# Kernel optimization log

Hardware: AMD Instinct MI355X
Metric: run time of the kernel (lower is better)

## Reference

```python
import jax, jax.numpy as jnp
import numpy as np

SEQ_LEN = 2048
NUM_HEADS = 16
BATCH = 2
HEAD_DIM = 64


def setup_inputs() -> dict:
    key = jax.random.key(0)
    k_q, k_e1, k_e2 = jax.random.split(key, 3)
    q = jax.random.normal(k_q, (BATCH * NUM_HEADS, SEQ_LEN, HEAD_DIM), dtype=jnp.float32)
    e1 = jax.random.normal(k_e1, (SEQ_LEN, NUM_HEADS), dtype=jnp.float32)
    e2 = jax.random.normal(k_e2, (SEQ_LEN - 1, NUM_HEADS), dtype=jnp.float32)
    return {"q": q, "e1": e1, "e2": e2}


def reference(q, e1, e2):
    # The original double loop of overwriting scatters reduces to:
    #   ret[i, j] = e1[i - j]      if i >= j   (delta = i - j in [0, S-1])
    #   ret[i, j] = e2[j - i - 1]  if j > i    (j - i - 1 in [0, S-2])
    seq_len = e1.shape[0]
    num_heads = e1.shape[1]
    batch_x_heads = q.shape[0]
    batch_dim = batch_x_heads // num_heads

    i = jnp.arange(seq_len)[:, None]
    j = jnp.arange(seq_len)[None, :]
    delta = i - j  # (S, S)
    idx1 = jnp.clip(delta, 0, seq_len - 1)
    idx2 = jnp.clip(-delta - 1, 0, seq_len - 2)
    # (S, S, H): gather from e1 below/on diagonal, e2 above diagonal
    bias = jnp.where((delta >= 0)[:, :, None], e1[idx1], e2[idx2])
    bias = jnp.transpose(bias, (2, 0, 1))  # (H, S, S)
    ret = jnp.tile(bias, (batch_dim, 1, 1))  # (B*H, S, S)
    return ret
```

## Files before the change

### kernel.cpp

```cpp
#include <hip/hip_runtime.h>

#define S    2048
#define H    16
#define ROWS 32
#define TPB  256
#define TILES_PER_H (S / ROWS)

typedef float f32x4 __attribute__((ext_vector_type(4)));

__global__ __launch_bounds__(TPB) void relpos_kernel(
    const float* __restrict__ e1,
    const float* __restrict__ e2,
    float* __restrict__ out)
{
    __shared__ __align__(16) float R[2 * S];

    const int tile = blockIdx.x & (TILES_PER_H - 1);
    const int h    = blockIdx.x >> 6;
    const int tid  = threadIdx.x;

    for (int v = tid; v < 2 * S - 1; v += TPB) {
        float val;
        if (v <= S - 1) val = e1[(S - 1 - v) * H + h];
        else            val = e2[(v - S) * H + h];
        R[v] = val;
    }
    __syncthreads();

    const int ibase = tile * ROWS;
    float* const out0 = out + (size_t)h * S * S + (size_t)ibase * S;
    float* const out1 = out0 + (size_t)H * S * S;

    #pragma unroll
    for (int k = 0; k < 2; ++k) {
        const int j0    = (tid + k * TPB) * 4;
        const int wbase = (S - 1 - ibase) + j0 - 31;
        f32x4 w4[9];
        #pragma unroll
        for (int c = 0; c < 9; ++c)
            w4[c] = *(const f32x4*)&R[wbase + 4 * c];
#define W(t) w4[(t) >> 2][(t) & 3]
        #pragma unroll
        for (int r = 0; r < ROWS; ++r) {
            f32x4 v;
            v.x = W(31 - r);
            v.y = W(32 - r);
            v.z = W(33 - r);
            v.w = W(34 - r);
            *(f32x4*)(out0 + (size_t)r * S + j0) = v;
            *(f32x4*)(out1 + (size_t)r * S + j0) = v;
        }
#undef W
    }
}

extern "C" void kernel_launch(void* const* d_in, const int* in_sizes, int n_in,
                              void* d_out, int out_size, void* d_ws, size_t ws_size,
                              hipStream_t stream) {
    const float* e1 = (const float*)d_in[1];
    const float* e2 = (const float*)d_in[2];
    float* out = (float*)d_out;

    const int grid = H * TILES_PER_H;
    relpos_kernel<<<grid, TPB, 0, stream>>>(e1, e2, out);
}
```

Baseline: 107.4 us.

## Split into prep kernel building per-head diagonal table and store-only main kernel

A small prep kernel now gathers the strided e1/e2 columns into a contiguous per-head table in workspace. The main kernel reads its window straight from that table in global memory, with no shared memory and no block-wide barrier. It launches one block per (batch*head, tile) and writes a single copy per block instead of two. This removes the redundant strided gather that every block repeated and doubles the grid for more parallelism, at the cost of an extra kernel launch and a dependency on workspace memory.

After: 105.7 us. No clear change (-1.6%).

```diff
diff --git a/kernel.cpp b/kernel.cpp
--- a/kernel.cpp
+++ b/kernel.cpp
@@ -5,31 +5,38 @@
 #define ROWS 32
 #define TPB  256
 #define TILES_PER_H (S / ROWS)
+#define MSTRIDE 4096
 
 typedef float f32x4 __attribute__((ext_vector_type(4)));
 
-__global__ __launch_bounds__(TPB) void relpos_kernel(
+
+__global__ __launch_bounds__(TPB) void relpos_prep(
     const float* __restrict__ e1,
     const float* __restrict__ e2,
+    float* __restrict__ M)
+{
+    const int h = blockIdx.x;
+    float* Mh = M + (size_t)h * MSTRIDE;
+    for (int v = threadIdx.x; v < MSTRIDE; v += TPB) {
+        float val = 0.0f;
+        if (v <= S - 1)          val = e1[(S - 1 - v) * H + h];
+        else if (v <= 2 * S - 2) val = e2[(v - S) * H + h];
+        Mh[v] = val;
+    }
+}
+
+__global__ __launch_bounds__(TPB) void relpos_main(
+    const float* __restrict__ M,
     float* __restrict__ out)
 {
-    __shared__ __align__(16) float R[2 * S];
-
     const int tile = blockIdx.x & (TILES_PER_H - 1);
-    const int h    = blockIdx.x >> 6;
+    const int bh   = blockIdx.x >> 6;
+    const int h    = bh & (H - 1);
     const int tid  = threadIdx.x;
 
-    for (int v = tid; v < 2 * S - 1; v += TPB) {
-        float val;
-        if (v <= S - 1) val = e1[(S - 1 - v) * H + h];
-        else            val = e2[(v - S) * H + h];
-        R[v] = val;
-    }
-    __syncthreads();
-
     const int ibase = tile * ROWS;
-    float* const out0 = out + (size_t)h * S * S + (size_t)ibase * S;
-    float* const out1 = out0 + (size_t)H * S * S;
+    const float* Mh = M + (size_t)h * MSTRIDE;
+    float* const o  = out + (size_t)bh * S * S + (size_t)ibase * S;
 
     #pragma unroll
     for (int k = 0; k < 2; ++k) {
@@ -38,7 +45,7 @@
         f32x4 w4[9];
         #pragma unroll
         for (int c = 0; c < 9; ++c)
-            w4[c] = *(const f32x4*)&R[wbase + 4 * c];
+            w4[c] = *(const f32x4*)&Mh[wbase + 4 * c];
 #define W(t) w4[(t) >> 2][(t) & 3]
         #pragma unroll
         for (int r = 0; r < ROWS; ++r) {
@@ -47,8 +54,7 @@
             v.y = W(32 - r);
             v.z = W(33 - r);
             v.w = W(34 - r);
-            *(f32x4*)(out0 + (size_t)r * S + j0) = v;
-            *(f32x4*)(out1 + (size_t)r * S + j0) = v;
+            *(f32x4*)(o + (size_t)r * S + j0) = v;
         }
 #undef W
     }
@@ -60,7 +66,8 @@
     const float* e1 = (const float*)d_in[1];
     const float* e2 = (const float*)d_in[2];
     float* out = (float*)d_out;
+    float* M   = (float*)d_ws;
 
-    const int grid = H * TILES_PER_H;
-    relpos_kernel<<<grid, TPB, 0, stream>>>(e1, e2, out);
+    relpos_prep<<<H, TPB, 0, stream>>>(e1, e2, M);
+    relpos_main<<<2 * H * TILES_PER_H, TPB, 0, stream>>>(M, out);
 }
```
